# Optimization experiments

Measured on AMD Instinct MI355X. Metric: run time of the kernel, lower is better.

## Reference

```python
import jax, jax.numpy as jnp
import numpy as np

NUM_EMBEDDINGS = 512
EMBEDDING_DIM = 64
COMMITMENT_COST = 0.25


def setup_inputs() -> dict:
    key = jax.random.key(0)
    k1, k2 = jax.random.split(key)
    inputs = jax.random.normal(k1, (32, 64, 64, 64), dtype=jnp.float32)  # NCHW, C=D
    # torch init: uniform(-1/K, 1/K)
    embeddings = jax.random.uniform(
        k2, (NUM_EMBEDDINGS, EMBEDDING_DIM), dtype=jnp.float32,
        minval=-1.0 / NUM_EMBEDDINGS, maxval=1.0 / NUM_EMBEDDINGS)
    return {"inputs": inputs, "embeddings": embeddings}


def reference(inputs, embeddings):
    # NCHW -> NHWC
    x = jnp.transpose(inputs, (0, 2, 3, 1))
    B, H, W, D = x.shape
    flat = x.reshape(-1, D)  # [N, D]
    # squared L2 distances to codebook: [N, K]
    distances = (jnp.sum(flat * flat, axis=1, keepdims=True)
                 + jnp.sum(embeddings * embeddings, axis=1)
                 - 2.0 * flat @ embeddings.T)
    encoding_indices = jnp.argmin(distances, axis=1)  # [N]
    # one-hot @ codebook in the original == direct gather
    quantized = embeddings[encoding_indices].reshape(B, H, W, D)
    # commitment loss (quantized is detached in original)
    e_latent_loss = jnp.mean((jax.lax.stop_gradient(quantized) - x) ** 2)
    loss = COMMITMENT_COST * e_latent_loss
    # straight-through estimator
    quantized_st = x + jax.lax.stop_gradient(quantized - x)
    out = jnp.transpose(quantized_st, (0, 3, 1, 2))  # back to NCHW
    return out, loss, encoding_indices.reshape(B, H, W)
```

## Files before the change

kernel.cpp:

```cpp
#include <hip/hip_runtime.h>
#include <math.h>

#define NUM_K 512
#define DIM   64
#define HW    4096
#define IMG   (DIM * HW)
#define OUT_Q 8388608
#define LOSS_OFF OUT_Q
#define IDX_OFF (OUT_Q + 1)
#define DELTA 8e-5f

#define WS_EH   0
#define WS_EL   65536
#define WS_SE   131072
#define WS_CNT  133120
#define WS_PART 133376
#define WS_ET   137472
#define WS_WL   268544

typedef float f32x4 __attribute__((ext_vector_type(4)));
typedef short s8v   __attribute__((ext_vector_type(8)));

__device__ inline short f2bf(float f) {
  unsigned u = __float_as_uint(f);
  return (short)((u + 0x7FFF + ((u >> 16) & 1)) >> 16);
}
__device__ inline float bf2f(short s) {
  return __uint_as_float(((unsigned)(unsigned short)s) << 16);
}

__global__ void vq_prep(const float* __restrict__ emb, char* __restrict__ ws) {
  short* eh = (short*)(ws + WS_EH);
  short* el = (short*)(ws + WS_EL);
  float* se = (float*)(ws + WS_SE);
  float* et = (float*)(ws + WS_ET);
  const int k = blockIdx.x * 256 + threadIdx.x;
  if (k == 0) *(int*)(ws + WS_CNT) = 0;
  const float* e = emb + k * DIM;
  float s = 0.f;
#pragma unroll
  for (int j = 0; j < DIM; ++j) {
    const float v = e[j];
    s = fmaf(v, v, s);
    const short h = f2bf(v);
    eh[k * DIM + j] = h;
    el[k * DIM + j] = f2bf(v - bf2f(h));
    et[j * NUM_K + k] = v;
  }
  se[k] = s;
}

__launch_bounds__(256, 2)
__global__ void vq_main(const float* __restrict__ in, const float* __restrict__ emb,
                        char* __restrict__ ws, float* __restrict__ out,
                        int wlcap, int wxcap, unsigned long long wxoff) {
  const short* eh = (const short*)(ws + WS_EH);
  const short* el = (const short*)(ws + WS_EL);
  const float* se = (const float*)(ws + WS_SE);
  int* wcnt  = (int*)(ws + WS_CNT);
  int* wlist = (int*)(ws + WS_WL);
  float* wx  = (float*)(ws + wxoff);
  double* partial = (double*)(ws + WS_PART);
  __shared__ int bkbuf[256];
  __shared__ int slotbuf[256];
  __shared__ unsigned char flg[256];
  __shared__ double red[4];

  const int tid = threadIdx.x;
  const int lane = tid & 63, w = tid >> 6;
  const int l15 = lane & 15, lh = lane >> 4;
  const int d0 = lh * 8;
  const int pblk = blockIdx.x * 256;
  const int n = pblk >> 12;
  const int hwb = pblk & 4095;
  const int p0 = w * 64;

  s8v ah[4][2], al[4][2];
#pragma unroll
  for (int rt = 0; rt < 4; ++rt) {
    const float* xp = in + (size_t)n * IMG + hwb + (p0 + rt * 16 + l15);
#pragma unroll
    for (int h = 0; h < 2; ++h) {
      s8v vh, vl;
#pragma unroll
      for (int j = 0; j < 8; ++j) {
        const float xv = xp[(h * 32 + d0 + j) * HW];
        const short hi = f2bf(xv);
        vh[j] = hi;
        vl[j] = f2bf(xv - bf2f(hi));
      }
      ah[rt][h] = vh; al[rt][h] = vl;
    }
  }

  float m1[4][4], m2[4][4];
#pragma unroll
  for (int rt = 0; rt < 4; ++rt)
#pragma unroll
    for (int r = 0; r < 4; ++r) { m1[rt][r] = INFINITY; m2[rt][r] = INFINITY; }

  for (int ct = 0; ct < 32; ++ct) {
    const int c = ct * 16 + l15;
    const s8v beh0 = *(const s8v*)(eh + c * DIM + d0);
    const s8v beh1 = *(const s8v*)(eh + c * DIM + 32 + d0);
    const s8v bel0 = *(const s8v*)(el + c * DIM + d0);
    const s8v bel1 = *(const s8v*)(el + c * DIM + 32 + d0);
    const float sec = se[c];
#pragma unroll
    for (int rt = 0; rt < 4; ++rt) {
      f32x4 acc = {0.f, 0.f, 0.f, 0.f};
      acc = __builtin_amdgcn_mfma_f32_16x16x32_bf16(ah[rt][0], beh0, acc, 0, 0, 0);
      acc = __builtin_amdgcn_mfma_f32_16x16x32_bf16(ah[rt][1], beh1, acc, 0, 0, 0);
      acc = __builtin_amdgcn_mfma_f32_16x16x32_bf16(al[rt][0], beh0, acc, 0, 0, 0);
      acc = __builtin_amdgcn_mfma_f32_16x16x32_bf16(al[rt][1], beh1, acc, 0, 0, 0);
      acc = __builtin_amdgcn_mfma_f32_16x16x32_bf16(ah[rt][0], bel0, acc, 0, 0, 0);
      acc = __builtin_amdgcn_mfma_f32_16x16x32_bf16(ah[rt][1], bel1, acc, 0, 0, 0);
#pragma unroll
      for (int r = 0; r < 4; ++r) {
        const float cv = fmaf(-2.f, acc[r], sec);
        const float pk = __int_as_float((__float_as_int(cv) & 0xFFFFFE00) | c);
        m2[rt][r] = fminf(m2[rt][r], fmaxf(m1[rt][r], pk));
        m1[rt][r] = fminf(m1[rt][r], pk);
      }
    }
  }

#pragma unroll
  for (int s = 1; s < 16; s <<= 1) {
#pragma unroll
    for (int rt = 0; rt < 4; ++rt)
#pragma unroll
      for (int r = 0; r < 4; ++r) {
        const float o1 = __shfl_xor(m1[rt][r], s);
        const float o2 = __shfl_xor(m2[rt][r], s);
        const float hi = fmaxf(m1[rt][r], o1);
        m1[rt][r] = fminf(m1[rt][r], o1);
        m2[rt][r] = fminf(fminf(m2[rt][r], o2), hi);
      }
  }
  if (l15 == 0) {
#pragma unroll
    for (int rt = 0; rt < 4; ++rt)
#pragma unroll
      for (int r = 0; r < 4; ++r) {
        const int lp = p0 + rt * 16 + lh * 4 + r;
        bkbuf[lp] = __float_as_int(m1[rt][r]) & 511;
        flg[lp] = (m2[rt][r] - m1[rt][r] <= DELTA) ? 1 : 0;
      }
  }
  __syncthreads();

  {
    const bool f = flg[tid] != 0;
    const unsigned long long b = __ballot(f);
    const int cnt = __popcll(b);
    int base = 0;
    if (cnt) {
      if (lane == 0) base = atomicAdd(wcnt, cnt);
      base = __shfl(base, 0);
    }
    int sl = -1;
    if (f) {
      const int pos = base + __popcll(b & ((1ull << lane) - 1));
      if (pos < wlcap) { sl = pos; wlist[pos] = pblk + tid; }
    }
    slotbuf[tid] = sl;
  }
  __syncthreads();

  float ls = 0.f;
#pragma unroll
  for (int rt = 0; rt < 4; ++rt) {
    const int lp = p0 + rt * 16 + l15;
    const int bk = bkbuf[lp];
    const int sl = slotbuf[lp];
    if (lh == 0) out[IDX_OFF + pblk + lp] = (float)bk;
    const float* ep = emb + bk * DIM;
    const float* xp = in  + (size_t)n * IMG + hwb + lp;
    float*       op = out + (size_t)n * IMG + hwb + lp;
#pragma unroll
    for (int h = 0; h < 2; ++h)
#pragma unroll
      for (int j = 0; j < 8; ++j) {
        const int d = h * 32 + d0 + j;
        const float q = ep[d];
        const float xv = xp[d * HW];
        op[d * HW] = q;
        if (sl >= 0 && sl < wxcap) wx[(size_t)sl * DIM + d] = xv;
        const float dd = q - xv;
        ls = fmaf(dd, dd, ls);
      }
  }
  double dls = (double)ls;
#pragma unroll
  for (int o = 32; o; o >>= 1) dls += __shfl_down(dls, o);
  if (lane == 0) red[w] = dls;
  __syncthreads();
  if (tid == 0) partial[blockIdx.x] = red[0] + red[1] + red[2] + red[3];
}

__launch_bounds__(512)
__global__ void vq_fix(const float* __restrict__ in, const float* __restrict__ emb,
                       char* __restrict__ ws, float* __restrict__ out,
                       int wlcap, int wxcap, unsigned long long wxoff) {
  const float* se = (const float*)(ws + WS_SE);
  const float* et = (const float*)(ws + WS_ET);
  const int* wlist = (const int*)(ws + WS_WL);
  const float* wx = (const float*)(ws + wxoff);
  double* partial = (double*)(ws + WS_PART);
  __shared__ float xs[DIM];
  __shared__ float pd[8];
  __shared__ int   pkk[8];
  __shared__ int   sbk;

  const int tid = threadIdx.x;
  const int lane = tid & 63, w = tid >> 6;
  int M = *(const int*)(ws + WS_CNT);
  if (M > wlcap) M = wlcap;

  for (int i = blockIdx.x; i < M; i += gridDim.x) {
    const int p = wlist[i];
    const int n = p >> 12, hw = p & 4095;
    if (tid < DIM) {
      xs[tid] = (i < wxcap) ? wx[(size_t)i * DIM + tid]
                            : in[(size_t)n * IMG + (size_t)tid * HW + hw];
    }
    __syncthreads();

    float sx = 0.f, a = 0.f;
#pragma unroll 8
    for (int j = 0; j < DIM; ++j) {
      const float xj = xs[j];
      sx = fmaf(xj, xj, sx);
      a  = fmaf(xj, et[j * NUM_K + tid], a);
    }
    float bd = (sx + se[tid]) - 2.f * a;
    int bki = tid;
#pragma unroll
    for (int s = 1; s < 64; s <<= 1) {
      const float od = __shfl_xor(bd, s);
      const int   oi = __shfl_xor(bki, s);
      const bool t = (od < bd) || (od == bd && oi < bki);
      bd = t ? od : bd; bki = t ? oi : bki;
    }
    if (lane == 0) { pd[w] = bd; pkk[w] = bki; }
    __syncthreads();
    if (tid == 0) {
      float fb = pd[0]; int fk = pkk[0];
#pragma unroll
      for (int q = 1; q < 8; ++q) {
        if (pd[q] < fb) { fb = pd[q]; fk = pkk[q]; }
      }
      sbk = fk;
    }
    __syncthreads();
    const int bkn = sbk;
    const int oldk = (int)out[IDX_OFF + p];
    if (bkn != oldk) {
      if (tid < DIM) {
        const float xj = xs[tid];
        const float qn = emb[bkn  * DIM + tid];
        const float qo = emb[oldk * DIM + tid];
        out[(size_t)n * IMG + (size_t)tid * HW + hw] = qn;
        const float dl = (qn - xj) * (qn - xj) - (qo - xj) * (qo - xj);
        double dd = (double)dl;
#pragma unroll
        for (int o = 32; o; o >>= 1) dd += __shfl_down(dd, o);
        if (tid == 0) {
          atomicAdd(&partial[0], dd);
          out[IDX_OFF + p] = (float)bkn;
        }
      }
    }
    __syncthreads();
  }
}

__global__ void vq_loss(const double* __restrict__ partial, float* __restrict__ out) {
  __shared__ double r2[4];
  const int tid = threadIdx.x;
  double s = partial[tid] + partial[tid + 256];
#pragma unroll
  for (int o = 32; o; o >>= 1) s += __shfl_down(s, o);
  if ((tid & 63) == 0) r2[tid >> 6] = s;
  __syncthreads();
  if (tid == 0) {
    const double t = r2[0] + r2[1] + r2[2] + r2[3];
    out[LOSS_OFF] = (float)(0.25 * t / (double)OUT_Q);
  }
}

extern "C" void kernel_launch(void* const* d_in, const int* in_sizes, int n_in,
                              void* d_out, int out_size, void* d_ws, size_t ws_size,
                              hipStream_t stream) {
  (void)in_sizes; (void)n_in; (void)out_size;
  const float* in  = (const float*)d_in[0];
  const float* emb = (const float*)d_in[1];
  float* out = (float*)d_out;
  char* ws = (char*)d_ws;
  size_t avail = ws_size > WS_WL ? ws_size - WS_WL : 0;
  int wlcap = (int)(avail / 4 < 131072 ? avail / 4 : 131072);
  unsigned long long wxoff = WS_WL + (unsigned long long)wlcap * 4;
  size_t avail2 = ws_size > wxoff ? ws_size - wxoff : 0;
  size_t wxc = avail2 / (DIM * 4);
  int wxcap = (int)(wxc < (size_t)wlcap ? wxc : (size_t)wlcap);
  vq_prep<<<2,    256, 0, stream>>>(emb, ws);
  vq_main<<<512,  256, 0, stream>>>(in, emb, ws, out, wlcap, wxcap, wxoff);
  vq_fix <<<2048, 512, 0, stream>>>(in, emb, ws, out, wlcap, wxcap, wxoff);
  vq_loss<<<1,    256, 0, stream>>>((const double*)(ws + WS_PART), out);
}
```

Before: 169.7 us.

## Split codebook across two wave groups and reuse split-bf16 registers for loss

```diff
diff --git a/kernel.cpp b/kernel.cpp
--- a/kernel.cpp
+++ b/kernel.cpp
@@ -34,13 +34,19 @@
   short* el = (short*)(ws + WS_EL);
   float* se = (float*)(ws + WS_SE);
   float* et = (float*)(ws + WS_ET);
-  const int k = blockIdx.x * 256 + threadIdx.x;
-  if (k == 0) *(int*)(ws + WS_CNT) = 0;
-  const float* e = emb + k * DIM;
+  __shared__ float ebuf[64][65];
+  const int tid = threadIdx.x;
+  const int kb  = blockIdx.x * 64;
+  if (blockIdx.x == 0 && tid == 0) *(int*)(ws + WS_CNT) = 0;
+#pragma unroll
+  for (int i = 0; i < 64; ++i)
+    ebuf[i][tid] = emb[(size_t)(kb + i) * DIM + tid];
+  __syncthreads();
+  const int k = kb + tid;
   float s = 0.f;
 #pragma unroll
   for (int j = 0; j < DIM; ++j) {
-    const float v = e[j];
+    const float v = ebuf[tid][j];
     s = fmaf(v, v, s);
     const short h = f2bf(v);
     eh[k * DIM + j] = h;
@@ -50,30 +56,29 @@
   se[k] = s;
 }
 
-__launch_bounds__(256, 2)
+__launch_bounds__(512, 4)
 __global__ void vq_main(const float* __restrict__ in, const float* __restrict__ emb,
-                        char* __restrict__ ws, float* __restrict__ out,
-                        int wlcap, int wxcap, unsigned long long wxoff) {
+                        char* __restrict__ ws, float* __restrict__ out, int wlcap) {
   const short* eh = (const short*)(ws + WS_EH);
   const short* el = (const short*)(ws + WS_EL);
   const float* se = (const float*)(ws + WS_SE);
   int* wcnt  = (int*)(ws + WS_CNT);
   int* wlist = (int*)(ws + WS_WL);
-  float* wx  = (float*)(ws + wxoff);
   double* partial = (double*)(ws + WS_PART);
-  __shared__ int bkbuf[256];
-  __shared__ int slotbuf[256];
-  __shared__ unsigned char flg[256];
-  __shared__ double red[4];
-
-  const int tid = threadIdx.x;
+  __shared__ float m1s[2][256], m2s[2][256];
+  __shared__ int   bkbuf[256];
+  __shared__ double red[8];
+
+  const int tid  = threadIdx.x;
   const int lane = tid & 63, w = tid >> 6;
+  const int side = w >> 2;
+  const int wq   = w & 3;
   const int l15 = lane & 15, lh = lane >> 4;
   const int d0 = lh * 8;
   const int pblk = blockIdx.x * 256;
   const int n = pblk >> 12;
   const int hwb = pblk & 4095;
-  const int p0 = w * 64;
+  const int p0 = wq * 64;
 
   s8v ah[4][2], al[4][2];
 #pragma unroll
@@ -99,8 +104,8 @@
 #pragma unroll
     for (int r = 0; r < 4; ++r) { m1[rt][r] = INFINITY; m2[rt][r] = INFINITY; }
 
-  for (int ct = 0; ct < 32; ++ct) {
-    const int c = ct * 16 + l15;
+  for (int ct = 0; ct < 16; ++ct) {
+    const int c = side * 256 + ct * 16 + l15;
     const s8v beh0 = *(const s8v*)(eh + c * DIM + d0);
     const s8v beh1 = *(const s8v*)(eh + c * DIM + 32 + d0);
     const s8v bel0 = *(const s8v*)(el + c * DIM + d0);
@@ -144,27 +149,30 @@
 #pragma unroll
       for (int r = 0; r < 4; ++r) {
         const int lp = p0 + rt * 16 + lh * 4 + r;
-        bkbuf[lp] = __float_as_int(m1[rt][r]) & 511;
-        flg[lp] = (m2[rt][r] - m1[rt][r] <= DELTA) ? 1 : 0;
-      }
-  }
-  __syncthreads();
-
-  {
-    const bool f = flg[tid] != 0;
-    const unsigned long long b = __ballot(f);
+        m1s[side][lp] = m1[rt][r];
+        m2s[side][lp] = m2[rt][r];
+      }
+  }
+  __syncthreads();
+
+  if (tid < 256) {
+    const float m1a = m1s[0][tid], m1b = m1s[1][tid];
+    const float m2a = m2s[0][tid], m2b = m2s[1][tid];
+    const float mm1 = fminf(m1a, m1b);
+    const float mm2 = fminf(fminf(m2a, m2b), fmaxf(m1a, m1b));
+    const int bk = __float_as_int(mm1) & 511;
+    bkbuf[tid] = bk;
+    out[IDX_OFF + pblk + tid] = (float)bk;
+    const int flagv = (mm2 - mm1 <= DELTA) ? 1 : 0;
+    const unsigned long long b = __ballot(flagv);
     const int cnt = __popcll(b);
     int base = 0;
-    if (cnt) {
-      if (lane == 0) base = atomicAdd(wcnt, cnt);
-      base = __shfl(base, 0);
-    }
-    int sl = -1;
-    if (f) {
+    if (lane == 0 && cnt) base = atomicAdd(wcnt, cnt);
+    base = __shfl(base, 0);
+    if (flagv) {
       const int pos = base + __popcll(b & ((1ull << lane) - 1));
-      if (pos < wlcap) { sl = pos; wlist[pos] = pblk + tid; }
-    }
-    slotbuf[tid] = sl;
+      if (pos < wlcap) wlist[pos] = pblk + tid;
+    }
   }
   __syncthreads();
 
@@ -173,40 +181,39 @@
   for (int rt = 0; rt < 4; ++rt) {
     const int lp = p0 + rt * 16 + l15;
     const int bk = bkbuf[lp];
-    const int sl = slotbuf[lp];
-    if (lh == 0) out[IDX_OFF + pblk + lp] = (float)bk;
-    const float* ep = emb + bk * DIM;
-    const float* xp = in  + (size_t)n * IMG + hwb + lp;
-    float*       op = out + (size_t)n * IMG + hwb + lp;
-#pragma unroll
-    for (int h = 0; h < 2; ++h)
-#pragma unroll
-      for (int j = 0; j < 8; ++j) {
-        const int d = h * 32 + d0 + j;
-        const float q = ep[d];
-        const float xv = xp[d * HW];
-        op[d * HW] = q;
-        if (sl >= 0 && sl < wxcap) wx[(size_t)sl * DIM + d] = xv;
-        const float dd = q - xv;
-        ls = fmaf(dd, dd, ls);
-      }
+    const float* ep = emb + bk * DIM + side * 32 + d0;
+    const f32x4 q0 = *(const f32x4*)ep;
+    const f32x4 q1 = *(const f32x4*)(ep + 4);
+    float* op = out + (size_t)n * IMG + (size_t)(side * 32 + d0) * HW + hwb + lp;
+    const s8v vh = ah[rt][side], vl = al[rt][side];
+#pragma unroll
+    for (int j = 0; j < 8; ++j) {
+      const float q = (j < 4) ? q0[j] : q1[j - 4];
+      op[j * HW] = q;
+      const float xv = bf2f(vh[j]) + bf2f(vl[j]);
+      const float dd = q - xv;
+      ls = fmaf(dd, dd, ls);
+    }
   }
   double dls = (double)ls;
 #pragma unroll
   for (int o = 32; o; o >>= 1) dls += __shfl_down(dls, o);
   if (lane == 0) red[w] = dls;
   __syncthreads();
-  if (tid == 0) partial[blockIdx.x] = red[0] + red[1] + red[2] + red[3];
+  if (tid == 0) {
+    double t = 0.0;
+#pragma unroll
+    for (int q = 0; q < 8; ++q) t += red[q];
+    partial[blockIdx.x] = t;
+  }
 }
 
 __launch_bounds__(512)
 __global__ void vq_fix(const float* __restrict__ in, const float* __restrict__ emb,
-                       char* __restrict__ ws, float* __restrict__ out,
-                       int wlcap, int wxcap, unsigned long long wxoff) {
+                       char* __restrict__ ws, float* __restrict__ out, int wlcap) {
   const float* se = (const float*)(ws + WS_SE);
   const float* et = (const float*)(ws + WS_ET);
   const int* wlist = (const int*)(ws + WS_WL);
-  const float* wx = (const float*)(ws + wxoff);
   double* partial = (double*)(ws + WS_PART);
   __shared__ float xs[DIM];
   __shared__ float pd[8];
@@ -221,10 +228,8 @@
   for (int i = blockIdx.x; i < M; i += gridDim.x) {
     const int p = wlist[i];
     const int n = p >> 12, hw = p & 4095;
-    if (tid < DIM) {
-      xs[tid] = (i < wxcap) ? wx[(size_t)i * DIM + tid]
-                            : in[(size_t)n * IMG + (size_t)tid * HW + hw];
-    }
+    if (tid < DIM)
+      xs[tid] = in[(size_t)n * IMG + (size_t)tid * HW + hw];
     __syncthreads();
 
     float sx = 0.f, a = 0.f;
@@ -248,28 +253,25 @@
     if (tid == 0) {
       float fb = pd[0]; int fk = pkk[0];
 #pragma unroll
-      for (int q = 1; q < 8; ++q) {
+      for (int q = 1; q < 8; ++q)
         if (pd[q] < fb) { fb = pd[q]; fk = pkk[q]; }
-      }
       sbk = fk;
     }
     __syncthreads();
     const int bkn = sbk;
     const int oldk = (int)out[IDX_OFF + p];
-    if (bkn != oldk) {
-      if (tid < DIM) {
-        const float xj = xs[tid];
-        const float qn = emb[bkn  * DIM + tid];
-        const float qo = emb[oldk * DIM + tid];
-        out[(size_t)n * IMG + (size_t)tid * HW + hw] = qn;
-        const float dl = (qn - xj) * (qn - xj) - (qo - xj) * (qo - xj);
-        double dd = (double)dl;
-#pragma unroll
-        for (int o = 32; o; o >>= 1) dd += __shfl_down(dd, o);
-        if (tid == 0) {
-          atomicAdd(&partial[0], dd);
-          out[IDX_OFF + p] = (float)bkn;
-        }
+    if (bkn != oldk && tid < DIM) {
+      const float xj = xs[tid];
+      const float qn = emb[bkn  * DIM + tid];
+      const float qo = emb[oldk * DIM + tid];
+      out[(size_t)n * IMG + (size_t)tid * HW + hw] = qn;
+      const float dl = (qn - xj) * (qn - xj) - (qo - xj) * (qo - xj);
+      double dd = (double)dl;
+#pragma unroll
+      for (int o = 32; o; o >>= 1) dd += __shfl_down(dd, o);
+      if (tid == 0) {
+        atomicAdd(&partial[0], dd);
+        out[IDX_OFF + p] = (float)bkn;
       }
     }
     __syncthreads();
@@ -300,12 +302,8 @@
   char* ws = (char*)d_ws;
   size_t avail = ws_size > WS_WL ? ws_size - WS_WL : 0;
   int wlcap = (int)(avail / 4 < 131072 ? avail / 4 : 131072);
-  unsigned long long wxoff = WS_WL + (unsigned long long)wlcap * 4;
-  size_t avail2 = ws_size > wxoff ? ws_size - wxoff : 0;
-  size_t wxc = avail2 / (DIM * 4);
-  int wxcap = (int)(wxc < (size_t)wlcap ? wxc : (size_t)wlcap);
-  vq_prep<<<2,    256, 0, stream>>>(emb, ws);
-  vq_main<<<512,  256, 0, stream>>>(in, emb, ws, out, wlcap, wxcap, wxoff);
-  vq_fix <<<2048, 512, 0, stream>>>(in, emb, ws, out, wlcap, wxcap, wxoff);
+  vq_prep<<<8,    64,  0, stream>>>(emb, ws);
+  vq_main<<<512,  512, 0, stream>>>(in, emb, ws, out, wlcap);
+  vq_fix <<<2048, 512, 0, stream>>>(in, emb, ws, out, wlcap);
   vq_loss<<<1,    256, 0, stream>>>((const double*)(ws + WS_PART), out);
 }
```

After: 191.7 us. 1.13x slower.
